# Kernel optimization log

Measured on AMD Instinct MI355X. Metric: run time of the kernel, lower is better.

## Reference

```python
import jax, jax.numpy as jnp
import numpy as np

N = 100000   # nodes
E = 1600000  # edges
D = 128      # input_dim == hidden_dim
L = 3        # n_layers
P = 7        # n_properties
B = 64       # graphs in batch
BN_EPS = 1e-5
NEG_SLOPE = 0.2


def setup_inputs() -> dict:
    key = jax.random.key(0)
    ks = jax.random.split(key, 18)
    s = 1.0 / np.sqrt(D)
    sp = 1.0 / np.sqrt(P)
    return {
        "x": jax.random.normal(ks[0], (N, D), jnp.float32),
        "edge_index": jax.random.randint(ks[1], (2, E), 0, N, dtype=jnp.int64),
        "batch": jnp.sort(jax.random.randint(ks[2], (N,), 0, B, dtype=jnp.int64)),
        "graph_stats": jax.random.normal(ks[3], (B, P), jnp.float32),
        # GIN MLP params (stacked over layers; input_dim == hidden_dim == D)
        "W1s": jax.random.normal(ks[4], (L, D, D), jnp.float32) * s,
        "b1s": jnp.zeros((L, D), jnp.float32),
        "gammas": jnp.ones((L, D), jnp.float32),
        "betas": jnp.zeros((L, D), jnp.float32),
        "bn_means": jax.random.normal(ks[5], (L, D), jnp.float32) * 0.1,
        "bn_vars": jax.random.uniform(ks[6], (L, D), jnp.float32) + 0.5,
        "W2s": jax.random.normal(ks[7], (L, D, D), jnp.float32) * s,
        "b2s": jnp.zeros((L, D), jnp.float32),
        # stat conditioning transforms
        "statWs": jax.random.normal(ks[8], (L, P, D), jnp.float32) * sp,
        "statBs": jnp.zeros((L, D), jnp.float32),
        # fc_out
        "fcW": jax.random.normal(ks[9], (D, D), jnp.float32) * s,
        "fcB": jnp.zeros((D,), jnp.float32),
    }


def reference(x, edge_index, batch, graph_stats,
              W1s, b1s, gammas, betas, bn_means, bn_vars, W2s, b2s,
              statWs, statBs, fcW, fcB):
    # per-node graph stats (nan -> -100, then broadcast by graph id)
    node_stats = jnp.nan_to_num(graph_stats, nan=-100.0)[batch]  # [N, P]
    src, dst = edge_index[0], edge_index[1]
    h = x
    for i in range(L):
        # GIN aggregation (eps = 0): (1+eps)*h_i + sum_{j->i} h_j
        agg = jax.ops.segment_sum(h[src], dst, num_segments=N)  # [N, D]
        m = h + agg
        # MLP: Linear -> LeakyReLU(0.2) -> BatchNorm1d (eval) -> Linear -> LeakyReLU(0.2)
        m = jax.nn.leaky_relu(m @ W1s[i] + b1s[i], NEG_SLOPE)
        m = (m - bn_means[i]) * (gammas[i] / jnp.sqrt(bn_vars[i] + BN_EPS)) + betas[i]
        m = jax.nn.leaky_relu(m @ W2s[i] + b2s[i], NEG_SLOPE)
        # stats conditioning add (dropout is identity in eval mode)
        h = m + node_stats @ statWs[i] + statBs[i]
    return h @ fcW + fcB  # [N, D]
```

## Files before the change

kernel.cpp:

```cpp
#include <hip/hip_runtime.h>
#include <math.h>

#define N_NODES 100000
#define N_EDGES 1600000
#define D 128
#define L_LAYERS 3
#define P_STATS 7
#define B_GRAPHS 64
#define BN_EPS 1e-5f
#define NEG_SLOPE 0.2f

#define NB 196
#define BCAP 10240
#define EPB 6400

typedef __attribute__((ext_vector_type(8))) short bf16x8;
typedef __attribute__((ext_vector_type(4))) float f32x4;

static __device__ __forceinline__ short f2bf(float f) {
    union { float f; unsigned u; } v;
    v.f = f;
    unsigned r = v.u + 0x7fffu + ((v.u >> 16) & 1u);
    return (short)(r >> 16);
}

static __device__ __forceinline__ float bf2f(short s) {
    union { unsigned u; float f; } v;
    v.u = ((unsigned)(unsigned short)s) << 16;
    return v.f;
}


__global__ void zero_n_kernel(int* __restrict__ p, int n) {
    int i = blockIdx.x * blockDim.x + threadIdx.x;
    if (i < n) p[i] = 0;
}

__global__ __launch_bounds__(256) void bucketA_kernel(const int* __restrict__ src,
                                                      const int* __restrict__ dst,
                                                      int* __restrict__ bucket_cnt,
                                                      int2* __restrict__ bucketbuf) {
    __shared__ int s_src[EPB];
    __shared__ int s_dst[EPB];
    __shared__ int hist[NB], base[NB], loc[NB];
    const int tid = threadIdx.x;
    const int e0 = blockIdx.x * EPB;
    for (int i = tid; i < NB; i += 256) { hist[i] = 0; loc[i] = 0; }
    __syncthreads();
    for (int i = tid; i < EPB; i += 256) {
        int s = src[e0 + i];
        int d = dst[e0 + i];
        s_src[i] = s;
        s_dst[i] = d;
        atomicAdd(&hist[d >> 9], 1);
    }
    __syncthreads();
    for (int i = tid; i < NB; i += 256)
        base[i] = hist[i] ? atomicAdd(&bucket_cnt[i], hist[i]) : 0;
    __syncthreads();
    for (int i = tid; i < EPB; i += 256) {
        int d = s_dst[i];
        int b = d >> 9;
        int off = atomicAdd(&loc[b], 1);
        int idx = base[b] + off;
        if (idx < BCAP) bucketbuf[(size_t)b * BCAP + idx] = make_int2(s_src[i], d);
    }
}

__global__ __launch_bounds__(256) void bucketB1_kernel(const int* __restrict__ bucket_cnt,
                                                       const int2* __restrict__ bucketbuf,
                                                       int* __restrict__ deg) {
    __shared__ int hist[512];
    const int b = blockIdx.x;
    for (int i = threadIdx.x; i < 512; i += 256) hist[i] = 0;
    __syncthreads();
    int cnt = min(bucket_cnt[b], BCAP);
    for (int i = threadIdx.x; i < cnt; i += 256) {
        int d = bucketbuf[(size_t)b * BCAP + i].y;
        atomicAdd(&hist[d & 511], 1);
    }
    __syncthreads();
    int nbase = b << 9;
    for (int i = threadIdx.x; i < 512; i += 256) {
        int node = nbase + i;
        if (node < N_NODES) deg[node] = hist[i];
    }
}

__global__ __launch_bounds__(256) void bucketB2_kernel(const int* __restrict__ bucket_cnt,
                                                       const int2* __restrict__ bucketbuf,
                                                       int* __restrict__ cursor,
                                                       int* __restrict__ csr_src) {
    const int b = blockIdx.x;
    int cnt = min(bucket_cnt[b], BCAP);
    for (int i = threadIdx.x; i < cnt; i += 256) {
        int2 p = bucketbuf[(size_t)b * BCAP + i];
        int pos = atomicAdd(&cursor[p.y], 1);
        csr_src[pos] = p.x;
    }
}


__global__ void scan1_kernel(const int* __restrict__ deg, int* __restrict__ incl,
                             int* __restrict__ bsum) {
    __shared__ int s[256];
    const int tid = threadIdx.x;
    const int base = blockIdx.x * 2048;
    int v[8];
    int sum = 0;
    const int idx0 = base + tid * 8;
#pragma unroll
    for (int i = 0; i < 8; ++i) {
        int idx = idx0 + i;
        int d = (idx < N_NODES) ? deg[idx] : 0;
        sum += d;
        v[i] = sum;
    }
    s[tid] = sum;
    __syncthreads();
    for (int off = 1; off < 256; off <<= 1) {
        int t = (tid >= off) ? s[tid - off] : 0;
        __syncthreads();
        s[tid] += t;
        __syncthreads();
    }
    int prev = (tid > 0) ? s[tid - 1] : 0;
#pragma unroll
    for (int i = 0; i < 8; ++i) {
        int idx = idx0 + i;
        if (idx < N_NODES) incl[idx] = v[i] + prev;
    }
    if (tid == 255) bsum[blockIdx.x] = s[255];
}

__global__ void scan2_kernel(int* __restrict__ bsum, int nb) {
    if (threadIdx.x == 0 && blockIdx.x == 0) {
        int run = 0;
        for (int i = 0; i < nb; ++i) { int t = bsum[i]; bsum[i] = run; run += t; }
    }
}

__global__ void scan3_kernel(const int* __restrict__ deg, const int* __restrict__ incl,
                             const int* __restrict__ bsum, int* __restrict__ start,
                             int* __restrict__ cursor) {
    int i = blockIdx.x * blockDim.x + threadIdx.x;
    if (i < N_NODES) {
        int inc = incl[i] + bsum[i >> 11];
        int st = inc - deg[i];
        start[i] = st;
        cursor[i] = st;
    }
    if (i == 0) start[N_NODES] = N_EDGES;
}

__global__ void gproj_kernel(const float* __restrict__ gs, const float* __restrict__ statWs,
                             const float* __restrict__ statBs, float* __restrict__ gproj) {
    int b = blockIdx.x;
    int l = blockIdx.y;
    int j = threadIdx.x;
    float acc = statBs[l * D + j];
#pragma unroll
    for (int p = 0; p < P_STATS; ++p) {
        float g = gs[b * P_STATS + p];
        if (g != g) g = -100.0f;
        acc += g * statWs[(l * P_STATS + p) * D + j];
    }
    gproj[(l * B_GRAPHS + b) * D + j] = acc;
}

__global__ void wconv_kernel(const float* __restrict__ W1s, const float* __restrict__ W2s,
                             const float* __restrict__ fcW, short* __restrict__ wt) {
    int mid = blockIdx.y;
    const float* src = (mid < 3) ? (W1s + mid * D * D)
                                 : ((mid < 6) ? (W2s + (mid - 3) * D * D) : fcW);
    short* dstm = wt + mid * D * D;
    int i = blockIdx.x * 256 + threadIdx.x;
    int k = i >> 7, n = i & 127;
    dstm[n * D + k] = f2bf(src[i]);
}

__global__ __launch_bounds__(256) void xconv_kernel(const float* __restrict__ x,
                                                    short* __restrict__ xb) {
    int i = blockIdx.x * 256 + threadIdx.x;
    const float4* x4 = (const float4*)x;
    float4 a = x4[i * 2], b = x4[i * 2 + 1];
    short s[8];
    s[0] = f2bf(a.x); s[1] = f2bf(a.y); s[2] = f2bf(a.z); s[3] = f2bf(a.w);
    s[4] = f2bf(b.x); s[5] = f2bf(b.y); s[6] = f2bf(b.z); s[7] = f2bf(b.w);
    *(bf16x8*)&xb[i * 8] = *(bf16x8*)s;
}

__global__ __launch_bounds__(256) void agg_kernel(const short* __restrict__ hb,
                                                  const int* __restrict__ start,
                                                  const int* __restrict__ csr_src,
                                                  short* __restrict__ m_bf) {
    int node = blockIdx.x * 16 + (threadIdx.x >> 4);
    int c8 = threadIdx.x & 15;
    const bf16x8* h8 = (const bf16x8*)hb;

    bf16x8 own = h8[node * 16 + c8];
    float acc[8];
#pragma unroll
    for (int i = 0; i < 8; ++i) acc[i] = bf2f(own[i]);

    int s = start[node];
    int e = start[node + 1];
    int k = s;
    for (; k + 4 <= e; k += 4) {
        int sn0 = csr_src[k];
        int sn1 = csr_src[k + 1];
        int sn2 = csr_src[k + 2];
        int sn3 = csr_src[k + 3];
        bf16x8 v0 = h8[sn0 * 16 + c8];
        bf16x8 v1 = h8[sn1 * 16 + c8];
        bf16x8 v2 = h8[sn2 * 16 + c8];
        bf16x8 v3 = h8[sn3 * 16 + c8];
#pragma unroll
        for (int i = 0; i < 8; ++i) acc[i] += bf2f(v0[i]);
#pragma unroll
        for (int i = 0; i < 8; ++i) acc[i] += bf2f(v1[i]);
#pragma unroll
        for (int i = 0; i < 8; ++i) acc[i] += bf2f(v2[i]);
#pragma unroll
        for (int i = 0; i < 8; ++i) acc[i] += bf2f(v3[i]);
    }
    for (; k < e; ++k) {
        int sn0 = csr_src[k];
        bf16x8 v0 = h8[sn0 * 16 + c8];
#pragma unroll
        for (int i = 0; i < 8; ++i) acc[i] += bf2f(v0[i]);
    }

    short pk[8];
#pragma unroll
    for (int i = 0; i < 8; ++i) pk[i] = f2bf(acc[i]);
    *(bf16x8*)&m_bf[node * D + c8 * 8] = *(bf16x8*)pk;
}

template <bool FUSE_FC>
__global__ __launch_bounds__(256, FUSE_FC ? 2 : 4) void mlp_mfma_kernel(
    const short* __restrict__ m_bf,
    const short* __restrict__ W1t,
    const float* __restrict__ b1,
    const float* __restrict__ gamma, const float* __restrict__ beta,
    const float* __restrict__ mean, const float* __restrict__ var,
    const short* __restrict__ W2t,
    const float* __restrict__ b2,
    const float* __restrict__ gproj, const int* __restrict__ batch,
    const short* __restrict__ Wft, const float* __restrict__ fcb,
    float* __restrict__ outf, short* __restrict__ outb) {
    __shared__ short sy[128 * 128];
    __shared__ float sB1[128], sSc[128], sSb[128], sB2[128], sFC[128];

    const int tid = threadIdx.x;
    const int wid = tid >> 6;
    const int lane = tid & 63;
    const int lr = lane & 15;
    const int lk = lane >> 4;

    if (tid < 128) {
        sB1[tid] = b1[tid];
        float sc = gamma[tid] * rsqrtf(var[tid] + BN_EPS);
        sSc[tid] = sc;
        sSb[tid] = beta[tid] - mean[tid] * sc;
        sB2[tid] = b2[tid];
        if (FUSE_FC) sFC[tid] = fcb[tid];
    }
    __syncthreads();

    const int nodeBase = blockIdx.x * 128 + (wid & 1) * 64;
    const int featBase = (wid >> 1) * 64;
    const int nlBase = (wid & 1) * 64;

    int nIdx[4];
#pragma unroll
    for (int mt = 0; mt < 4; ++mt) {
        int n = nodeBase + mt * 16 + lr;
        nIdx[mt] = (n < N_NODES) ? n : (N_NODES - 1);
    }

    f32x4 acc[4][4];
#pragma unroll
    for (int ft = 0; ft < 4; ++ft)
#pragma unroll
        for (int mt = 0; mt < 4; ++mt)
            acc[ft][mt] = (f32x4)(0.0f);

#pragma unroll
    for (int kt = 0; kt < 4; ++kt) {
        bf16x8 wfk[4];
#pragma unroll
        for (int ft = 0; ft < 4; ++ft)
            wfk[ft] = *(const bf16x8*)&W1t[(featBase + ft * 16 + lr) * D + kt * 32 + lk * 8];
        bf16x8 mf[4];
#pragma unroll
        for (int mt = 0; mt < 4; ++mt)
            mf[mt] = *(const bf16x8*)&m_bf[nIdx[mt] * D + kt * 32 + lk * 8];
#pragma unroll
        for (int ft = 0; ft < 4; ++ft)
#pragma unroll
            for (int mt = 0; mt < 4; ++mt)
                acc[ft][mt] = __builtin_amdgcn_mfma_f32_16x16x32_bf16(wfk[ft], mf[mt],
                                                                      acc[ft][mt], 0, 0, 0);
    }

#pragma unroll
    for (int ft = 0; ft < 4; ++ft) {
        int f0 = featBase + ft * 16 + lk * 4;
#pragma unroll
        for (int mt = 0; mt < 4; ++mt) {
            int nl = nlBase + mt * 16 + lr;
            short4 pk;
#pragma unroll
            for (int r = 0; r < 4; ++r) {
                float v = acc[ft][mt][r] + sB1[f0 + r];
                v = (v > 0.f) ? v : NEG_SLOPE * v;
                v = v * sSc[f0 + r] + sSb[f0 + r];
                ((short*)&pk)[r] = f2bf(v);
            }
            int byteoff = nl * 256 + f0 * 2;
            byteoff ^= (nl & 7) << 4;
            *(short4*)((char*)sy + byteoff) = pk;
        }
    }
    __syncthreads();

#pragma unroll
    for (int ft = 0; ft < 4; ++ft)
#pragma unroll
        for (int mt = 0; mt < 4; ++mt)
            acc[ft][mt] = (f32x4)(0.0f);

#pragma unroll
    for (int kt = 0; kt < 4; ++kt) {
        bf16x8 wfk[4];
#pragma unroll
        for (int ft = 0; ft < 4; ++ft)
            wfk[ft] = *(const bf16x8*)&W2t[(featBase + ft * 16 + lr) * D + kt * 32 + lk * 8];
        bf16x8 yf[4];
#pragma unroll
        for (int mt = 0; mt < 4; ++mt) {
            int nl = nlBase + mt * 16 + lr;
            int byteoff = nl * 256 + kt * 64 + lk * 16;
            byteoff ^= (nl & 7) << 4;
            yf[mt] = *(const bf16x8*)((char*)sy + byteoff);
        }
#pragma unroll
        for (int ft = 0; ft < 4; ++ft)
#pragma unroll
            for (int mt = 0; mt < 4; ++mt)
                acc[ft][mt] = __builtin_amdgcn_mfma_f32_16x16x32_bf16(wfk[ft], yf[mt],
                                                                      acc[ft][mt], 0, 0, 0);
    }

    if (!FUSE_FC) {
#pragma unroll
        for (int mt = 0; mt < 4; ++mt) {
            int node = nodeBase + mt * 16 + lr;
            if (node >= N_NODES) continue;
            int bid = batch[node];
#pragma unroll
            for (int ft = 0; ft < 4; ++ft) {
                int f0 = featBase + ft * 16 + lk * 4;
                const float4 gp = *(const float4*)&gproj[bid * D + f0];
                float v0 = acc[ft][mt][0] + sB2[f0 + 0]; v0 = (v0 > 0.f) ? v0 : NEG_SLOPE * v0; v0 += gp.x;
                float v1 = acc[ft][mt][1] + sB2[f0 + 1]; v1 = (v1 > 0.f) ? v1 : NEG_SLOPE * v1; v1 += gp.y;
                float v2 = acc[ft][mt][2] + sB2[f0 + 2]; v2 = (v2 > 0.f) ? v2 : NEG_SLOPE * v2; v2 += gp.z;
                float v3 = acc[ft][mt][3] + sB2[f0 + 3]; v3 = (v3 > 0.f) ? v3 : NEG_SLOPE * v3; v3 += gp.w;
                short4 pk;
                pk.x = f2bf(v0); pk.y = f2bf(v1); pk.z = f2bf(v2); pk.w = f2bf(v3);
                *(short4*)&outb[node * D + f0] = pk;
            }
        }
        return;
    }

    __syncthreads();
#pragma unroll
    for (int ft = 0; ft < 4; ++ft) {
        int f0 = featBase + ft * 16 + lk * 4;
#pragma unroll
        for (int mt = 0; mt < 4; ++mt) {
            int nl = nlBase + mt * 16 + lr;
            int bid = batch[nIdx[mt]];
            const float4 gp = *(const float4*)&gproj[bid * D + f0];
            short4 pk;
            float v0 = acc[ft][mt][0] + sB2[f0 + 0]; v0 = (v0 > 0.f) ? v0 : NEG_SLOPE * v0; v0 += gp.x;
            float v1 = acc[ft][mt][1] + sB2[f0 + 1]; v1 = (v1 > 0.f) ? v1 : NEG_SLOPE * v1; v1 += gp.y;
            float v2 = acc[ft][mt][2] + sB2[f0 + 2]; v2 = (v2 > 0.f) ? v2 : NEG_SLOPE * v2; v2 += gp.z;
            float v3 = acc[ft][mt][3] + sB2[f0 + 3]; v3 = (v3 > 0.f) ? v3 : NEG_SLOPE * v3; v3 += gp.w;
            pk.x = f2bf(v0); pk.y = f2bf(v1); pk.z = f2bf(v2); pk.w = f2bf(v3);
            int byteoff = nl * 256 + f0 * 2;
            byteoff ^= (nl & 7) << 4;
            *(short4*)((char*)sy + byteoff) = pk;
        }
    }
    __syncthreads();

#pragma unroll
    for (int ft = 0; ft < 4; ++ft)
#pragma unroll
        for (int mt = 0; mt < 4; ++mt)
            acc[ft][mt] = (f32x4)(0.0f);

#pragma unroll
    for (int kt = 0; kt < 4; ++kt) {
        bf16x8 wfk[4];
#pragma unroll
        for (int ft = 0; ft < 4; ++ft)
            wfk[ft] = *(const bf16x8*)&Wft[(featBase + ft * 16 + lr) * D + kt * 32 + lk * 8];
        bf16x8 hf[4];
#pragma unroll
        for (int mt = 0; mt < 4; ++mt) {
            int nl = nlBase + mt * 16 + lr;
            int byteoff = nl * 256 + kt * 64 + lk * 16;
            byteoff ^= (nl & 7) << 4;
            hf[mt] = *(const bf16x8*)((char*)sy + byteoff);
        }
#pragma unroll
        for (int ft = 0; ft < 4; ++ft)
#pragma unroll
            for (int mt = 0; mt < 4; ++mt)
                acc[ft][mt] = __builtin_amdgcn_mfma_f32_16x16x32_bf16(wfk[ft], hf[mt],
                                                                      acc[ft][mt], 0, 0, 0);
    }

#pragma unroll
    for (int mt = 0; mt < 4; ++mt) {
        int node = nodeBase + mt * 16 + lr;
        if (node >= N_NODES) continue;
#pragma unroll
        for (int ft = 0; ft < 4; ++ft) {
            int f0 = featBase + ft * 16 + lk * 4;
            float4 o;
            o.x = acc[ft][mt][0] + sFC[f0 + 0];
            o.y = acc[ft][mt][1] + sFC[f0 + 1];
            o.z = acc[ft][mt][2] + sFC[f0 + 2];
            o.w = acc[ft][mt][3] + sFC[f0 + 3];
            *(float4*)&outf[node * D + f0] = o;
        }
    }
}


extern "C" void kernel_launch(void* const* d_in, const int* in_sizes, int n_in,
                              void* d_out, int out_size, void* d_ws, size_t ws_size,
                              hipStream_t stream) {
    const float* x = (const float*)d_in[0];
    const int* ei = (const int*)d_in[1];
    const int* src = ei;
    const int* dst = ei + N_EDGES;
    const int* batch = (const int*)d_in[2];
    const float* gs = (const float*)d_in[3];
    const float* W1s = (const float*)d_in[4];
    const float* b1s = (const float*)d_in[5];
    const float* gammas = (const float*)d_in[6];
    const float* betas = (const float*)d_in[7];
    const float* means = (const float*)d_in[8];
    const float* vars = (const float*)d_in[9];
    const float* W2s = (const float*)d_in[10];
    const float* b2s = (const float*)d_in[11];
    const float* statWs = (const float*)d_in[12];
    const float* statBs = (const float*)d_in[13];
    const float* fcW = (const float*)d_in[14];
    const float* fcB = (const float*)d_in[15];
    float* out = (float*)d_out;

    char* ws = (char*)d_ws;
    auto alloc = [&](size_t bytes) {
        char* p = ws;
        ws += (bytes + 255) / 256 * 256;
        return p;
    };
    int* deg = (int*)alloc(N_NODES * sizeof(int));
    int* incl = (int*)alloc(N_NODES * sizeof(int));
    int* bsum = (int*)alloc(64 * sizeof(int));
    int* start = (int*)alloc((N_NODES + 1) * sizeof(int));
    int* cursor = (int*)alloc(N_NODES * sizeof(int));
    int* csr_src = (int*)alloc(N_EDGES * sizeof(int));
    int* bucket_cnt = (int*)alloc(NB * sizeof(int));
    int2* bucketbuf = (int2*)alloc((size_t)NB * BCAP * sizeof(int2));
    float* gproj = (float*)alloc((size_t)L_LAYERS * B_GRAPHS * D * sizeof(float));
    short* wt = (short*)alloc((size_t)7 * D * D * sizeof(short));
    short* xb = (short*)alloc((size_t)N_NODES * D * sizeof(short));
    short* hb = (short*)alloc((size_t)N_NODES * D * sizeof(short));
    short* m_bf = (short*)alloc((size_t)N_NODES * D * sizeof(short));

    const int nscan = (N_NODES + 2047) / 2048;

    zero_n_kernel<<<1, 256, 0, stream>>>(bucket_cnt, NB);
    bucketA_kernel<<<N_EDGES / EPB, 256, 0, stream>>>(src, dst, bucket_cnt, bucketbuf);
    bucketB1_kernel<<<NB, 256, 0, stream>>>(bucket_cnt, bucketbuf, deg);
    scan1_kernel<<<nscan, 256, 0, stream>>>(deg, incl, bsum);
    scan2_kernel<<<1, 64, 0, stream>>>(bsum, nscan);
    scan3_kernel<<<(N_NODES + 255) / 256, 256, 0, stream>>>(deg, incl, bsum, start, cursor);
    bucketB2_kernel<<<NB, 256, 0, stream>>>(bucket_cnt, bucketbuf, cursor, csr_src);

    gproj_kernel<<<dim3(B_GRAPHS, L_LAYERS), D, 0, stream>>>(gs, statWs, statBs, gproj);
    wconv_kernel<<<dim3(64, 7), 256, 0, stream>>>(W1s, W2s, fcW, wt);
    xconv_kernel<<<(N_NODES * D / 8 + 255) / 256, 256, 0, stream>>>(x, xb);

    const int agg_blocks = N_NODES / 16;
    const int mlp_blocks = (N_NODES + 127) / 128;

    agg_kernel<<<agg_blocks, 256, 0, stream>>>(xb, start, csr_src, m_bf);
    mlp_mfma_kernel<false><<<mlp_blocks, 256, 0, stream>>>(
        m_bf, wt + 0 * D * D, b1s + 0 * D, gammas + 0 * D, betas + 0 * D, means + 0 * D,
        vars + 0 * D, wt + 3 * D * D, b2s + 0 * D, gproj + 0 * B_GRAPHS * D, batch,
        nullptr, nullptr, nullptr, hb);
    agg_kernel<<<agg_blocks, 256, 0, stream>>>(hb, start, csr_src, m_bf);
    mlp_mfma_kernel<false><<<mlp_blocks, 256, 0, stream>>>(
        m_bf, wt + 1 * D * D, b1s + 1 * D, gammas + 1 * D, betas + 1 * D, means + 1 * D,
        vars + 1 * D, wt + 4 * D * D, b2s + 1 * D, gproj + 1 * B_GRAPHS * D, batch,
        nullptr, nullptr, nullptr, hb);
    agg_kernel<<<agg_blocks, 256, 0, stream>>>(hb, start, csr_src, m_bf);
    mlp_mfma_kernel<true><<<mlp_blocks, 256, 0, stream>>>(
        m_bf, wt + 2 * D * D, b1s + 2 * D, gammas + 2 * D, betas + 2 * D, means + 2 * D,
        vars + 2 * D, wt + 5 * D * D, b2s + 2 * D, gproj + 2 * B_GRAPHS * D, batch,
        wt + 6 * D * D, fcB, out, nullptr);
}
```

Baseline: 394.1 us.

## Fuse neighbor aggregation into MLP kernel via shared-memory staging

Drops the separate aggregation kernel. Each MLP block now gathers its own 128 nodes' neighbor sums into swizzled shared memory, and the first GEMM reads its operands from LDS instead of a global m_bf buffer. This removes a full N×D bf16 write and read per layer plus one launch per layer, and ping-pongs between two h buffers because the gather reads global h while outputs are written. The cost is gather parallelism tied to MLP block occupancy: 782 blocks, with launch bounds forced to 4 for the FC variant, which may leave too few waves in flight to hide the random gather latency.

```diff
diff --git a/kernel.cpp b/kernel.cpp
--- a/kernel.cpp
+++ b/kernel.cpp
@@ -190,56 +190,10 @@
     *(bf16x8*)&xb[i * 8] = *(bf16x8*)s;
 }
 
-__global__ __launch_bounds__(256) void agg_kernel(const short* __restrict__ hb,
-                                                  const int* __restrict__ start,
-                                                  const int* __restrict__ csr_src,
-                                                  short* __restrict__ m_bf) {
-    int node = blockIdx.x * 16 + (threadIdx.x >> 4);
-    int c8 = threadIdx.x & 15;
-    const bf16x8* h8 = (const bf16x8*)hb;
-
-    bf16x8 own = h8[node * 16 + c8];
-    float acc[8];
-#pragma unroll
-    for (int i = 0; i < 8; ++i) acc[i] = bf2f(own[i]);
-
-    int s = start[node];
-    int e = start[node + 1];
-    int k = s;
-    for (; k + 4 <= e; k += 4) {
-        int sn0 = csr_src[k];
-        int sn1 = csr_src[k + 1];
-        int sn2 = csr_src[k + 2];
-        int sn3 = csr_src[k + 3];
-        bf16x8 v0 = h8[sn0 * 16 + c8];
-        bf16x8 v1 = h8[sn1 * 16 + c8];
-        bf16x8 v2 = h8[sn2 * 16 + c8];
-        bf16x8 v3 = h8[sn3 * 16 + c8];
-#pragma unroll
-        for (int i = 0; i < 8; ++i) acc[i] += bf2f(v0[i]);
-#pragma unroll
-        for (int i = 0; i < 8; ++i) acc[i] += bf2f(v1[i]);
-#pragma unroll
-        for (int i = 0; i < 8; ++i) acc[i] += bf2f(v2[i]);
-#pragma unroll
-        for (int i = 0; i < 8; ++i) acc[i] += bf2f(v3[i]);
-    }
-    for (; k < e; ++k) {
-        int sn0 = csr_src[k];
-        bf16x8 v0 = h8[sn0 * 16 + c8];
-#pragma unroll
-        for (int i = 0; i < 8; ++i) acc[i] += bf2f(v0[i]);
-    }
-
-    short pk[8];
-#pragma unroll
-    for (int i = 0; i < 8; ++i) pk[i] = f2bf(acc[i]);
-    *(bf16x8*)&m_bf[node * D + c8 * 8] = *(bf16x8*)pk;
-}
-
 template <bool FUSE_FC>
-__global__ __launch_bounds__(256, FUSE_FC ? 2 : 4) void mlp_mfma_kernel(
-    const short* __restrict__ m_bf,
+__global__ __launch_bounds__(256, 4) void mlp_fused_kernel(
+    const short* __restrict__ h_in,
+    const int* __restrict__ start, const int* __restrict__ csr_src,
     const short* __restrict__ W1t,
     const float* __restrict__ b1,
     const float* __restrict__ gamma, const float* __restrict__ beta,
@@ -266,6 +220,59 @@
         sB2[tid] = b2[tid];
         if (FUSE_FC) sFC[tid] = fcb[tid];
     }
+
+    {
+        const bf16x8* h8 = (const bf16x8*)h_in;
+        const int c8 = lane & 15;
+        const int sub = lane >> 4;
+#pragma unroll
+        for (int it = 0; it < 8; ++it) {
+            int nl = wid * 32 + it * 4 + sub;
+            int node = blockIdx.x * 128 + nl;
+            float acc[8];
+            if (node < N_NODES) {
+                bf16x8 own = h8[node * 16 + c8];
+#pragma unroll
+                for (int i = 0; i < 8; ++i) acc[i] = bf2f(own[i]);
+                int s = start[node];
+                int e = start[node + 1];
+                int k = s;
+                for (; k + 4 <= e; k += 4) {
+                    int sn0 = csr_src[k];
+                    int sn1 = csr_src[k + 1];
+                    int sn2 = csr_src[k + 2];
+                    int sn3 = csr_src[k + 3];
+                    bf16x8 v0 = h8[sn0 * 16 + c8];
+                    bf16x8 v1 = h8[sn1 * 16 + c8];
+                    bf16x8 v2 = h8[sn2 * 16 + c8];
+                    bf16x8 v3 = h8[sn3 * 16 + c8];
+#pragma unroll
+                    for (int i = 0; i < 8; ++i) acc[i] += bf2f(v0[i]);
+#pragma unroll
+                    for (int i = 0; i < 8; ++i) acc[i] += bf2f(v1[i]);
+#pragma unroll
+                    for (int i = 0; i < 8; ++i) acc[i] += bf2f(v2[i]);
+#pragma unroll
+                    for (int i = 0; i < 8; ++i) acc[i] += bf2f(v3[i]);
+                }
+                for (; k < e; ++k) {
+                    int sn0 = csr_src[k];
+                    bf16x8 v0 = h8[sn0 * 16 + c8];
+#pragma unroll
+                    for (int i = 0; i < 8; ++i) acc[i] += bf2f(v0[i]);
+                }
+            } else {
+#pragma unroll
+                for (int i = 0; i < 8; ++i) acc[i] = 0.f;
+            }
+            short pk[8];
+#pragma unroll
+            for (int i = 0; i < 8; ++i) pk[i] = f2bf(acc[i]);
+            int byteoff = nl * 256 + c8 * 16;
+            byteoff ^= (nl & 7) << 4;
+            *(bf16x8*)((char*)sy + byteoff) = *(bf16x8*)pk;
+        }
+    }
     __syncthreads();
 
     const int nodeBase = blockIdx.x * 128 + (wid & 1) * 64;
@@ -294,8 +301,12 @@
             wfk[ft] = *(const bf16x8*)&W1t[(featBase + ft * 16 + lr) * D + kt * 32 + lk * 8];
         bf16x8 mf[4];
 #pragma unroll
-        for (int mt = 0; mt < 4; ++mt)
-            mf[mt] = *(const bf16x8*)&m_bf[nIdx[mt] * D + kt * 32 + lk * 8];
+        for (int mt = 0; mt < 4; ++mt) {
+            int nl = nlBase + mt * 16 + lr;
+            int byteoff = nl * 256 + kt * 64 + lk * 16;
+            byteoff ^= (nl & 7) << 4;
+            mf[mt] = *(const bf16x8*)((char*)sy + byteoff);
+        }
 #pragma unroll
         for (int ft = 0; ft < 4; ++ft)
 #pragma unroll
@@ -303,6 +314,7 @@
                 acc[ft][mt] = __builtin_amdgcn_mfma_f32_16x16x32_bf16(wfk[ft], mf[mt],
                                                                       acc[ft][mt], 0, 0, 0);
     }
+    __syncthreads();
 
 #pragma unroll
     for (int ft = 0; ft < 4; ++ft) {
@@ -483,8 +495,8 @@
     float* gproj = (float*)alloc((size_t)L_LAYERS * B_GRAPHS * D * sizeof(float));
     short* wt = (short*)alloc((size_t)7 * D * D * sizeof(short));
     short* xb = (short*)alloc((size_t)N_NODES * D * sizeof(short));
-    short* hb = (short*)alloc((size_t)N_NODES * D * sizeof(short));
-    short* m_bf = (short*)alloc((size_t)N_NODES * D * sizeof(short));
+    short* hb1 = (short*)alloc((size_t)N_NODES * D * sizeof(short));
+    short* hb2 = (short*)alloc((size_t)N_NODES * D * sizeof(short));
 
     const int nscan = (N_NODES + 2047) / 2048;
 
@@ -500,22 +512,18 @@
     wconv_kernel<<<dim3(64, 7), 256, 0, stream>>>(W1s, W2s, fcW, wt);
     xconv_kernel<<<(N_NODES * D / 8 + 255) / 256, 256, 0, stream>>>(x, xb);
 
-    const int agg_blocks = N_NODES / 16;
     const int mlp_blocks = (N_NODES + 127) / 128;
 
-    agg_kernel<<<agg_blocks, 256, 0, stream>>>(xb, start, csr_src, m_bf);
-    mlp_mfma_kernel<false><<<mlp_blocks, 256, 0, stream>>>(
-        m_bf, wt + 0 * D * D, b1s + 0 * D, gammas + 0 * D, betas + 0 * D, means + 0 * D,
-        vars + 0 * D, wt + 3 * D * D, b2s + 0 * D, gproj + 0 * B_GRAPHS * D, batch,
-        nullptr, nullptr, nullptr, hb);
-    agg_kernel<<<agg_blocks, 256, 0, stream>>>(hb, start, csr_src, m_bf);
-    mlp_mfma_kernel<false><<<mlp_blocks, 256, 0, stream>>>(
-        m_bf, wt + 1 * D * D, b1s + 1 * D, gammas + 1 * D, betas + 1 * D, means + 1 * D,
-        vars + 1 * D, wt + 4 * D * D, b2s + 1 * D, gproj + 1 * B_GRAPHS * D, batch,
-        nullptr, nullptr, nullptr, hb);
-    agg_kernel<<<agg_blocks, 256, 0, stream>>>(hb, start, csr_src, m_bf);
-    mlp_mfma_kernel<true><<<mlp_blocks, 256, 0, stream>>>(
-        m_bf, wt + 2 * D * D, b1s + 2 * D, gammas + 2 * D, betas + 2 * D, means + 2 * D,
-        vars + 2 * D, wt + 5 * D * D, b2s + 2 * D, gproj + 2 * B_GRAPHS * D, batch,
-        wt + 6 * D * D, fcB, out, nullptr);
-}
+    mlp_fused_kernel<false><<<mlp_blocks, 256, 0, stream>>>(
+        xb, start, csr_src, wt + 0 * D * D, b1s + 0 * D, gammas + 0 * D, betas + 0 * D,
+        means + 0 * D, vars + 0 * D, wt + 3 * D * D, b2s + 0 * D, gproj + 0 * B_GRAPHS * D,
+        batch, nullptr, nullptr, nullptr, hb1);
+    mlp_fused_kernel<false><<<mlp_blocks, 256, 0, stream>>>(
+        hb1, start, csr_src, wt + 1 * D * D, b1s + 1 * D, gammas + 1 * D, betas + 1 * D,
+        means + 1 * D, vars + 1 * D, wt + 4 * D * D, b2s + 1 * D, gproj + 1 * B_GRAPHS * D,
+        batch, nullptr, nullptr, nullptr, hb2);
+    mlp_fused_kernel<true><<<mlp_blocks, 256, 0, stream>>>(
+        hb2, start, csr_src, wt + 2 * D * D, b1s + 2 * D, gammas + 2 * D, betas + 2 * D,
+        means + 2 * D, vars + 2 * D, wt + 5 * D * D, b2s + 2 * D, gproj + 2 * B_GRAPHS * D,
+        batch, wt + 6 * D * D, fcB, out, nullptr);
+}
```

Result: faster. 380.5 us (-3.4%).
